# Kernel tuning notes

Hardware: AMD Instinct MI355X
Metric: run time of the kernel (lower is better)

Reference implementation:

```python
import jax, jax.numpy as jnp
import numpy as np

B, N, M, DIN, H = 8, 2048, 2048, 512, 256
SCALE = float(np.sqrt(H))


def _lin_params(key, din, dout):
    kw, kb = jax.random.split(key)
    lim = 1.0 / np.sqrt(din)
    W = jax.random.uniform(kw, (din, dout), jnp.float32, -lim, lim)
    b = jax.random.uniform(kb, (dout,), jnp.float32, -lim, lim)
    return W, b


def setup_inputs() -> dict:
    key = jax.random.key(0)
    ks = jax.random.split(key, 16)
    inp = {
        "q_fp": jax.random.normal(ks[0], (B, N, DIN), jnp.float32),
        "v_ret": jax.random.normal(ks[1], (B, M, DIN), jnp.float32),
        "pi_star": jax.random.uniform(ks[2], (B, N, M), jnp.float32),
    }
    names = ["qs", "ks", "vs", "qe", "ke", "ve"]
    for i, nm in enumerate(names):
        W, b = _lin_params(ks[3 + i], DIN, H)
        inp[f"W{nm}"], inp[f"b{nm}"] = W, b
    inp["W1"], inp["b1"] = _lin_params(ks[10], 4 * H, H)
    inp["W2"], inp["b2"] = _lin_params(ks[11], H, H)
    inp["gamma"] = jnp.ones((1,), jnp.float32)
    inp["ew"] = jnp.array(1.0, jnp.float32)
    return inp


def _forward(q_fp, v_ret, pi_star, Wqs, bqs, Wks, bks, Wvs, bvs,
             Wqe, bqe, Wke, bke, Wve, bve, W1, b1, W2, b2, gamma, ew):
    q_struct = q_fp @ Wqs + bqs          # [B,N,H]
    k_struct = v_ret @ Wks + bks         # [B,M,H]
    v_struct = v_ret @ Wvs + bvs
    q_elec = q_fp @ Wqe + bqe
    k_elec = v_ret @ Wke + bke
    v_elec = v_ret @ Wve + bve

    structural_logits = jnp.einsum("bnh,bmh->bnm", q_struct, k_struct) / SCALE

    # cdist(p=2) via the quadratic expansion, clamped for numeric safety
    q2 = jnp.sum(q_elec * q_elec, -1, keepdims=True)          # [B,N,1]
    k2 = jnp.sum(k_elec * k_elec, -1, keepdims=True)          # [B,M,1]
    d2 = q2 + jnp.swapaxes(k2, -2, -1) - 2.0 * jnp.einsum("bnh,bmh->bnm", q_elec, k_elec)
    electronic_distance = jnp.sqrt(jnp.maximum(d2, 1e-12))    # [B,N,M]
    electronic_scale = jnp.maximum(
        electronic_distance.mean(axis=(-2, -1), keepdims=True), 1e-4)
    electronic_logits = -(electronic_distance / electronic_scale)

    pi_mask = gamma * jnp.log(jnp.maximum(pi_star, 1e-9))
    final_logits = structural_logits + ew * electronic_logits + pi_mask
    attn = jax.nn.softmax(final_logits, axis=-1)              # [B,N,M]

    ctx_s = jnp.einsum("bnm,bmh->bnh", attn, v_struct)
    ctx_e = jnp.einsum("bnm,bmh->bnh", attn, v_elec)
    fused = jnp.concatenate([ctx_s, ctx_e, ctx_s - ctx_e, ctx_s * ctx_e], axis=-1)
    h = jax.nn.silu(fused @ W1 + b1)
    return h @ W2 + b2


def reference(q_fp, v_ret, pi_star, Wqs, bqs, Wks, bks, Wvs, bvs,
              Wqe, bqe, Wke, bke, Wve, bve, W1, b1, W2, b2, gamma, ew):
    return _forward(q_fp, v_ret, pi_star, Wqs, bqs, Wks, bks, Wvs, bvs,
                    Wqe, bqe, Wke, bke, Wve, bve, W1, b1, W2, b2, gamma, ew)
```

## Files before the change

kernel.cpp:

```cpp
#include <hip/hip_runtime.h>

#define Bsz 8
#define Nq  2048
#define Mk  2048
#define BKt 32

typedef __attribute__((ext_vector_type(8))) short   short8;
typedef __attribute__((ext_vector_type(4))) float   floatx4;

__device__ __forceinline__ unsigned short f2bf(float f) {
  union { float f; unsigned u; } x; x.f = f;
  unsigned r = x.u + 0x7fffu + ((x.u >> 16) & 1u);
  return (unsigned short)(r >> 16);
}
__device__ __forceinline__ float bf2f(unsigned short s) {
  union { unsigned u; float f; } x; x.u = ((unsigned)s) << 16;
  return x.f;
}

__device__ __forceinline__ void async16(const unsigned short* g, unsigned short* l) {
  __builtin_amdgcn_global_load_lds(
      (const __attribute__((address_space(1))) unsigned int*)g,
      (__attribute__((address_space(3))) unsigned int*)l, 16, 0, 0);
}

__device__ __forceinline__ void gemm_core_nt(
    const unsigned short* __restrict__ A, int lda,
    const unsigned short* __restrict__ B, int ldb,
    int K, unsigned short* ldsA, unsigned short* ldsB,
    floatx4 (&acc)[4][4])
{
  const int tid  = threadIdx.x;
  const int lane = tid & 63;
  const int sr   = tid >> 2;
  const int sc   = (tid & 3) << 3;
  const int wid  = tid >> 6;
  const int wm   = wid & 1;
  const int wn   = wid >> 1;
  const int fr   = lane & 15;
  const int fk   = (lane >> 4) << 3;

  const unsigned short* a0p = A + (size_t)sr * lda + sc;
  const unsigned short* a1p = A + (size_t)(sr + 64) * lda + sc;
  const unsigned short* b0p = B + (size_t)sr * ldb + sc;
  const unsigned short* b1p = B + (size_t)(sr + 64) * ldb + sc;
  unsigned short* la0 = ldsA + tid * 8;
  unsigned short* la1 = ldsA + 2048 + tid * 8;
  unsigned short* lb0 = ldsB + tid * 8;
  unsigned short* lb1 = ldsB + 2048 + tid * 8;
  const unsigned short* fa = ldsA + (wm * 64 + fr) * BKt + fk;
  const unsigned short* fb = ldsB + (wn * 64 + fr) * BKt + fk;

  for (int k0 = 0; k0 < K; k0 += BKt) {
    __syncthreads();
    async16(a0p, la0); a0p += BKt;
    async16(a1p, la1); a1p += BKt;
    async16(b0p, lb0); b0p += BKt;
    async16(b1p, lb1); b1p += BKt;
    __syncthreads();
    short8 af[4], bfr[4];
#pragma unroll
    for (int i = 0; i < 4; i++) af[i]  = *(const short8*)(fa + i * 16 * BKt);
#pragma unroll
    for (int i = 0; i < 4; i++) bfr[i] = *(const short8*)(fb + i * 16 * BKt);
#pragma unroll
    for (int i = 0; i < 4; i++)
#pragma unroll
      for (int j = 0; j < 4; j++)
        acc[i][j] = __builtin_amdgcn_mfma_f32_16x16x32_bf16(af[i], bfr[j], acc[i][j], 0, 0, 0);
  }
}

#define EPILOGUE_VARS \
  const int lane = threadIdx.x & 63; \
  const int wid  = threadIdx.x >> 6; \
  const int wm   = wid & 1; \
  const int wn   = wid >> 1; \
  const int r4   = (lane >> 4) * 4;  \
  const int cn   = lane & 15; \
  (void)wid;

template<int MODE>
__global__ __launch_bounds__(256) void k_gemm_bias(
    const unsigned short* __restrict__ A, const unsigned short* __restrict__ Bw,
    const float* __restrict__ bias, void* __restrict__ Cout, int Ncols, int K)
{
  __shared__ alignas(16) unsigned short ldsA[128 * BKt];
  __shared__ alignas(16) unsigned short ldsB[128 * BKt];
  floatx4 acc[4][4];
#pragma unroll
  for (int i = 0; i < 4; i++)
#pragma unroll
    for (int j = 0; j < 4; j++)
#pragma unroll
      for (int t = 0; t < 4; t++) acc[i][j][t] = 0.f;

  const unsigned short* Ab = A + (size_t)blockIdx.x * 128 * K;
  const unsigned short* Bb = Bw + (size_t)blockIdx.y * 128 * K;
  gemm_core_nt(Ab, K, Bb, K, K, ldsA, ldsB, acc);

  EPILOGUE_VARS
#pragma unroll
  for (int i = 0; i < 4; i++) {
#pragma unroll
    for (int j = 0; j < 4; j++) {
      int gc = blockIdx.y * 128 + wn * 64 + j * 16 + cn;
      float bv = bias[gc];
#pragma unroll
      for (int r = 0; r < 4; r++) {
        int gr = blockIdx.x * 128 + wm * 64 + i * 16 + r4 + r;
        float v = acc[i][j][r] + bv;
        if constexpr (MODE == 1) v = v / (1.f + __expf(-v));
        if constexpr (MODE == 2)
          ((float*)Cout)[(size_t)gr * Ncols + gc] = v;
        else
          ((unsigned short*)Cout)[(size_t)gr * Ncols + gc] = f2bf(v);
      }
    }
  }
}

__global__ __launch_bounds__(256) void k_pass1(
    const unsigned short* __restrict__ Xq, const unsigned short* __restrict__ Xk,
    const float* __restrict__ q2, const float* __restrict__ k2,
    float* __restrict__ dsum, float* __restrict__ rowsum)
{
  {
    int blin = (blockIdx.z * 16 + blockIdx.y) * 16 + blockIdx.x;
    if (threadIdx.x < 8) rowsum[blin * 8 + threadIdx.x] = 0.f;
  }
  __shared__ alignas(16) unsigned short ldsA[128 * BKt];
  __shared__ alignas(16) unsigned short ldsB[128 * BKt];
  floatx4 acc[4][4];
#pragma unroll
  for (int i = 0; i < 4; i++)
#pragma unroll
    for (int j = 0; j < 4; j++)
#pragma unroll
      for (int t = 0; t < 4; t++) acc[i][j][t] = 0.f;

  const int b = blockIdx.z;
  const unsigned short* Ab = Xq + ((size_t)(b * Nq) + blockIdx.x * 128) * 512 + 256;
  const unsigned short* Bb = Xk + ((size_t)(b * Mk) + blockIdx.y * 128) * 1024 + 512;
  gemm_core_nt(Ab, 512, Bb, 1024, 256, ldsA, ldsB, acc);

  EPILOGUE_VARS
  const int rowBase = b * Nq + blockIdx.x * 128;
  const int colBase = b * Mk + blockIdx.y * 128;
  float lsum = 0.f;
#pragma unroll
  for (int i = 0; i < 4; i++) {
#pragma unroll
    for (int j = 0; j < 4; j++) {
      float kk = k2[colBase + wn * 64 + j * 16 + cn];
#pragma unroll
      for (int r = 0; r < 4; r++) {
        float qq = q2[rowBase + wm * 64 + i * 16 + r4 + r];
        float d2 = qq + kk - 2.f * acc[i][j][r];
        lsum += sqrtf(fmaxf(d2, 1e-12f));
      }
    }
  }
#pragma unroll
  for (int o = 32; o; o >>= 1) lsum += __shfl_down(lsum, o);
  __syncthreads();
  float* red = (float*)ldsA;
  if (lane == 0) red[wid] = lsum;
  __syncthreads();
  if (threadIdx.x == 0) atomicAdd(dsum + b, red[0] + red[1] + red[2] + red[3]);
}

__global__ __launch_bounds__(256) void k_logits(
    const unsigned short* __restrict__ Xq, const unsigned short* __restrict__ Xk,
    const float* __restrict__ q2, const float* __restrict__ k2,
    const float* __restrict__ dsum, const float* __restrict__ pi,
    const float* __restrict__ gamma_p, const float* __restrict__ ew_p,
    unsigned short* __restrict__ attn, float* __restrict__ rowsum)
{
  __shared__ alignas(16) unsigned short ldsA[128 * BKt];
  __shared__ alignas(16) unsigned short ldsB[128 * BKt];
  floatx4 accS[4][4], accE[4][4];
#pragma unroll
  for (int i = 0; i < 4; i++)
#pragma unroll
    for (int j = 0; j < 4; j++)
#pragma unroll
      for (int t = 0; t < 4; t++) { accS[i][j][t] = 0.f; accE[i][j][t] = 0.f; }

  const int b = blockIdx.z;
  const unsigned short* Aq_s = Xq + ((size_t)(b * Nq) + blockIdx.x * 128) * 512;
  const unsigned short* Bk_s = Xk + ((size_t)(b * Mk) + blockIdx.y * 128) * 1024;
  gemm_core_nt(Aq_s,       512, Bk_s,       1024, 256, ldsA, ldsB, accS);
  gemm_core_nt(Aq_s + 256, 512, Bk_s + 512, 1024, 256, ldsA, ldsB, accE);

  const float scale = fmaxf(dsum[b] * (1.f / (2048.f * 2048.f)), 1e-4f);
  const float einv  = ew_p[0] / scale;
  const float gv    = gamma_p[0];

  EPILOGUE_VARS
  float rs[4][4];
#pragma unroll
  for (int i = 0; i < 4; i++)
#pragma unroll
    for (int r = 0; r < 4; r++) rs[i][r] = 0.f;

#pragma unroll
  for (int i = 0; i < 4; i++) {
#pragma unroll
    for (int j = 0; j < 4; j++) {
      int m = blockIdx.y * 128 + wn * 64 + j * 16 + cn;
      float kk = k2[b * Mk + m];
#pragma unroll
      for (int r = 0; r < 4; r++) {
        int n = blockIdx.x * 128 + wm * 64 + i * 16 + r4 + r;
        float qq = q2[b * Nq + n];
        float d  = sqrtf(fmaxf(qq + kk - 2.f * accE[i][j][r], 1e-12f));
        float p  = pi[((size_t)b * Nq + n) * Mk + m];
        float l  = accS[i][j][r] * 0.0625f - einv * d + gv * __logf(fmaxf(p, 1e-9f));
        float e  = __expf(l);
        rs[i][r] += e;
        attn[((size_t)b * Nq + n) * Mk + m] = f2bf(e);
      }
    }
  }
#pragma unroll
  for (int i = 0; i < 4; i++)
#pragma unroll
    for (int r = 0; r < 4; r++) {
      float v = rs[i][r];
      v += __shfl_xor(v, 1); v += __shfl_xor(v, 2);
      v += __shfl_xor(v, 4); v += __shfl_xor(v, 8);
      if (cn == 0)
        atomicAdd(rowsum + b * Nq + blockIdx.x * 128 + wm * 64 + i * 16 + r4 + r, v);
    }
}

__global__ __launch_bounds__(256) void k_pv(
    const unsigned short* __restrict__ At, const unsigned short* __restrict__ VT,
    const float* __restrict__ rowsum, unsigned short* __restrict__ ctx)
{
  __shared__ alignas(16) unsigned short ldsA[128 * BKt];
  __shared__ alignas(16) unsigned short ldsB[128 * BKt];
  floatx4 acc[4][4];
#pragma unroll
  for (int i = 0; i < 4; i++)
#pragma unroll
    for (int j = 0; j < 4; j++)
#pragma unroll
      for (int t = 0; t < 4; t++) acc[i][j][t] = 0.f;

  const int b = blockIdx.z;
  const unsigned short* Ab = At + ((size_t)b * Nq + blockIdx.x * 128) * (size_t)Mk;
  const unsigned short* Bb = VT + ((size_t)b * 512 + blockIdx.y * 128) * (size_t)Mk;
  gemm_core_nt(Ab, Mk, Bb, Mk, Mk, ldsA, ldsB, acc);

  EPILOGUE_VARS
  const int rowbase = b * Nq + blockIdx.x * 128 + wm * 64;
  float rinv[4][4];
#pragma unroll
  for (int i = 0; i < 4; i++)
#pragma unroll
    for (int r = 0; r < 4; r++)
      rinv[i][r] = 1.f / rowsum[rowbase + i * 16 + r4 + r];
#pragma unroll
  for (int i = 0; i < 4; i++)
#pragma unroll
    for (int j = 0; j < 4; j++) {
      int gc = blockIdx.y * 128 + wn * 64 + j * 16 + cn;
#pragma unroll
      for (int r = 0; r < 4; r++) {
        int gr = blockIdx.x * 128 + wm * 64 + i * 16 + r4 + r;
        ctx[((size_t)b * Nq + gr) * 512 + gc] = f2bf(acc[i][j][r] * rinv[i][r]);
      }
    }
}

__global__ void k_f32_bf16(const float* __restrict__ src, unsigned short* __restrict__ dst) {
  size_t i = ((size_t)blockIdx.x * 256 + threadIdx.x) * 4;
  float4 v = *(const float4*)(src + i);
  uint2 o;
  o.x = f2bf(v.x) | ((unsigned)f2bf(v.y) << 16);
  o.y = f2bf(v.z) | ((unsigned)f2bf(v.w) << 16);
  *(uint2*)(dst + i) = o;
}

__global__ void k_prep_w(
    const float* __restrict__ Wqs, const float* __restrict__ Wqe,
    const float* __restrict__ Wks, const float* __restrict__ Wvs,
    const float* __restrict__ Wke, const float* __restrict__ Wve,
    const float* __restrict__ W1,  const float* __restrict__ W2,
    const float* __restrict__ bqs, const float* __restrict__ bqe,
    const float* __restrict__ bks, const float* __restrict__ bvs,
    const float* __restrict__ bke, const float* __restrict__ bve,
    unsigned short* __restrict__ WqT, unsigned short* __restrict__ WkT,
    unsigned short* __restrict__ W1T, unsigned short* __restrict__ W2T,
    float* __restrict__ bq, float* __restrict__ bk, float* __restrict__ dsum)
{
  int gid = blockIdx.x * 256 + threadIdx.x;
  int idx = gid;
  if (idx < 512 * 512) {
    int j = idx >> 9, k = idx & 511;
    float v = (j < 256) ? Wqs[k * 256 + j] : Wqe[k * 256 + (j - 256)];
    WqT[idx] = f2bf(v);
  } else if ((idx -= 512 * 512) < 1024 * 512) {
    int j = idx >> 9, k = idx & 511;
    int s = j >> 8, jj = j & 255;
    const float* Wp = (s == 0) ? Wks : (s == 1) ? Wvs : (s == 2) ? Wke : Wve;
    WkT[idx] = f2bf(Wp[k * 256 + jj]);
  } else if ((idx -= 1024 * 512) < 256 * 1024) {
    int j = idx >> 10, k = idx & 1023;
    W1T[idx] = f2bf(W1[k * 256 + j]);
  } else if ((idx -= 256 * 1024) < 256 * 256) {
    int j = idx >> 8, k = idx & 255;
    W2T[idx] = f2bf(W2[k * 256 + j]);
  }
  if (gid < 512)  bq[gid] = (gid < 256) ? bqs[gid] : bqe[gid - 256];
  if (gid < 1024) bk[gid] = (gid < 256) ? bks[gid]
                    : (gid < 512) ? bvs[gid - 256]
                    : (gid < 768) ? bke[gid - 512] : bve[gid - 768];
  if (gid < 8) dsum[gid] = 0.f;
}

__global__ __launch_bounds__(256) void k_rowsq(
    const unsigned short* __restrict__ X, int stride, int colOff, float* __restrict__ out)
{
  int row = blockIdx.x * 4 + (threadIdx.x >> 6);
  int lane = threadIdx.x & 63;
  const unsigned short* p = X + (size_t)row * stride + colOff + lane * 4;
  uint2 u = *(const uint2*)p;
  float a0 = bf2f((unsigned short)(u.x & 0xffff));
  float a1 = bf2f((unsigned short)(u.x >> 16));
  float a2 = bf2f((unsigned short)(u.y & 0xffff));
  float a3 = bf2f((unsigned short)(u.y >> 16));
  float s = a0 * a0 + a1 * a1 + a2 * a2 + a3 * a3;
#pragma unroll
  for (int o = 32; o; o >>= 1) s += __shfl_down(s, o);
  if (lane == 0) out[row] = s;
}

__global__ void k_trans_vt(const unsigned short* __restrict__ Xk, unsigned short* __restrict__ VT) {
  __shared__ unsigned short t[32][33];
  const int b = blockIdx.z;
  const int m0 = blockIdx.x * 32, j0 = blockIdx.y * 32;
  const int tx = threadIdx.x, ty = threadIdx.y;
#pragma unroll
  for (int i = 0; i < 4; i++) {
    int m = m0 + ty + i * 8;
    int j = j0 + tx;
    int c = (j < 256) ? (256 + j) : (512 + j);
    t[ty + i * 8][tx] = Xk[((size_t)b * Mk + m) * 1024 + c];
  }
  __syncthreads();
#pragma unroll
  for (int i = 0; i < 4; i++) {
    int j = j0 + ty + i * 8;
    int m = m0 + tx;
    VT[((size_t)b * 512 + j) * Mk + m] = t[tx][ty + i * 8];
  }
}

__global__ void k_fused(const unsigned short* __restrict__ ctx, unsigned short* __restrict__ fused) {
  int idx = blockIdx.x * 256 + threadIdx.x;
  int bn = idx >> 8;
  int j = idx & 255;
  float cs = bf2f(ctx[(size_t)bn * 512 + j]);
  float ce = bf2f(ctx[(size_t)bn * 512 + 256 + j]);
  size_t o = (size_t)bn * 1024 + j;
  fused[o]       = f2bf(cs);
  fused[o + 256] = f2bf(ce);
  fused[o + 512] = f2bf(cs - ce);
  fused[o + 768] = f2bf(cs * ce);
}

extern "C" void kernel_launch(void* const* d_in, const int* in_sizes, int n_in,
                              void* d_out, int out_size, void* d_ws, size_t ws_size,
                              hipStream_t stream) {
  (void)in_sizes; (void)n_in; (void)out_size; (void)ws_size;
  const float* q_fp  = (const float*)d_in[0];
  const float* v_ret = (const float*)d_in[1];
  const float* pi    = (const float*)d_in[2];
  const float* Wqs = (const float*)d_in[3];  const float* bqs = (const float*)d_in[4];
  const float* Wks = (const float*)d_in[5];  const float* bks = (const float*)d_in[6];
  const float* Wvs = (const float*)d_in[7];  const float* bvs = (const float*)d_in[8];
  const float* Wqe = (const float*)d_in[9];  const float* bqe = (const float*)d_in[10];
  const float* Wke = (const float*)d_in[11]; const float* bke = (const float*)d_in[12];
  const float* Wve = (const float*)d_in[13]; const float* bve = (const float*)d_in[14];
  const float* W1  = (const float*)d_in[15]; const float* b1  = (const float*)d_in[16];
  const float* W2  = (const float*)d_in[17]; const float* b2  = (const float*)d_in[18];
  const float* gamma = (const float*)d_in[19];
  const float* ew    = (const float*)d_in[20];

  char* w = (char*)d_ws;
  unsigned short* WqT = (unsigned short*)(w + 0);
  unsigned short* WkT = (unsigned short*)(w + 524288);
  unsigned short* W1T = (unsigned short*)(w + 1572864);
  unsigned short* W2T = (unsigned short*)(w + 2097152);
  float* bq   = (float*)(w + 2228224);
  float* bk   = (float*)(w + 2230272);
  float* q2   = (float*)(w + 2234368);
  float* k2   = (float*)(w + 2299904);
  float* dsum = (float*)(w + 2365440);
  unsigned short* Aq = (unsigned short*)(w + 2365696);
  unsigned short* Ak = (unsigned short*)(w + 19142912);
  unsigned short* Xq = (unsigned short*)(w + 35920128);
  unsigned short* Xk = (unsigned short*)(w + 52697344);
  unsigned short* VT = (unsigned short*)(w + 86251776);
  unsigned short* attn = (unsigned short*)(w + 103028992);
  unsigned short* ctx  = Aq;
  unsigned short* fused = (unsigned short*)(w + 103028992);
  unsigned short* hbuf  = Ak;
  float* rowsum = (float*)d_out;

  k_f32_bf16<<<8192, 256, 0, stream>>>(q_fp, Aq);
  k_f32_bf16<<<8192, 256, 0, stream>>>(v_ret, Ak);
  k_prep_w<<<4352, 256, 0, stream>>>(Wqs, Wqe, Wks, Wvs, Wke, Wve, W1, W2,
                                     bqs, bqe, bks, bvs, bke, bve,
                                     WqT, WkT, W1T, W2T, bq, bk, dsum);
  k_gemm_bias<0><<<dim3(128, 4), 256, 0, stream>>>(Aq, WqT, bq, Xq, 512, 512);
  k_gemm_bias<0><<<dim3(128, 8), 256, 0, stream>>>(Ak, WkT, bk, Xk, 1024, 512);
  k_rowsq<<<4096, 256, 0, stream>>>(Xq, 512, 256, q2);
  k_rowsq<<<4096, 256, 0, stream>>>(Xk, 1024, 512, k2);
  k_pass1<<<dim3(16, 16, 8), 256, 0, stream>>>(Xq, Xk, q2, k2, dsum, rowsum);
  k_logits<<<dim3(16, 16, 8), 256, 0, stream>>>(Xq, Xk, q2, k2, dsum, pi, gamma, ew,
                                                attn, rowsum);
  k_trans_vt<<<dim3(64, 16, 8), dim3(32, 8), 0, stream>>>(Xk, VT);
  k_pv<<<dim3(16, 4, 8), 256, 0, stream>>>(attn, VT, rowsum, ctx);
  k_fused<<<16384, 256, 0, stream>>>(ctx, fused);
  k_gemm_bias<1><<<dim3(128, 2), 256, 0, stream>>>(fused, W1T, b1, hbuf, 256, 1024);
  k_gemm_bias<2><<<dim3(128, 2), 256, 0, stream>>>(hbuf, W2T, b2, d_out, 256, 256);
}
```

Before: 671.0 us.

## Cache electronic distances in fp16 from pass1 and drop recompute GEMM in logits

Pass1 now writes each computed cdist value as fp16 into the attention buffer, and the logits kernel reads it back instead of recomputing the electronic GEMM. This roughly halves the MFMA work in the logits kernel, which now relies on in-place aliasing of Dbuf and attn (each element is read before it is overwritten). The pi log/exp is skipped when gamma is 1, and the GEMM core swaps async global-to-LDS loads for register-staged loads issued before the barrier. It adds 2 bytes per element of extra HBM write and read and costs fp16 precision on the distances. Launch bounds with min 4 blocks per SM are also added.

New measurement: 609.9 us. 1.1x faster.

```diff
diff --git a/kernel.cpp b/kernel.cpp
--- a/kernel.cpp
+++ b/kernel.cpp
@@ -16,12 +16,6 @@
 __device__ __forceinline__ float bf2f(unsigned short s) {
   union { unsigned u; float f; } x; x.u = ((unsigned)s) << 16;
   return x.f;
-}
-
-__device__ __forceinline__ void async16(const unsigned short* g, unsigned short* l) {
-  __builtin_amdgcn_global_load_lds(
-      (const __attribute__((address_space(1))) unsigned int*)g,
-      (__attribute__((address_space(3))) unsigned int*)l, 16, 0, 0);
 }
 
 __device__ __forceinline__ void gemm_core_nt(
@@ -44,19 +38,20 @@
   const unsigned short* a1p = A + (size_t)(sr + 64) * lda + sc;
   const unsigned short* b0p = B + (size_t)sr * ldb + sc;
   const unsigned short* b1p = B + (size_t)(sr + 64) * ldb + sc;
-  unsigned short* la0 = ldsA + tid * 8;
-  unsigned short* la1 = ldsA + 2048 + tid * 8;
-  unsigned short* lb0 = ldsB + tid * 8;
-  unsigned short* lb1 = ldsB + 2048 + tid * 8;
+  uint4* sa0 = (uint4*)(ldsA + sr * BKt + sc);
+  uint4* sa1 = (uint4*)(ldsA + (sr + 64) * BKt + sc);
+  uint4* sb0 = (uint4*)(ldsB + sr * BKt + sc);
+  uint4* sb1 = (uint4*)(ldsB + (sr + 64) * BKt + sc);
   const unsigned short* fa = ldsA + (wm * 64 + fr) * BKt + fk;
   const unsigned short* fb = ldsB + (wn * 64 + fr) * BKt + fk;
 
   for (int k0 = 0; k0 < K; k0 += BKt) {
+    uint4 a0 = *(const uint4*)a0p; a0p += BKt;
+    uint4 a1 = *(const uint4*)a1p; a1p += BKt;
+    uint4 b0 = *(const uint4*)b0p; b0p += BKt;
+    uint4 b1 = *(const uint4*)b1p; b1p += BKt;
     __syncthreads();
-    async16(a0p, la0); a0p += BKt;
-    async16(a1p, la1); a1p += BKt;
-    async16(b0p, lb0); b0p += BKt;
-    async16(b1p, lb1); b1p += BKt;
+    *sa0 = a0; *sa1 = a1; *sb0 = b0; *sb1 = b1;
     __syncthreads();
     short8 af[4], bfr[4];
 #pragma unroll
@@ -120,10 +115,11 @@
   }
 }
 
-__global__ __launch_bounds__(256) void k_pass1(
+__global__ __launch_bounds__(256, 4) void k_pass1(
     const unsigned short* __restrict__ Xq, const unsigned short* __restrict__ Xk,
     const float* __restrict__ q2, const float* __restrict__ k2,
-    float* __restrict__ dsum, float* __restrict__ rowsum)
+    float* __restrict__ dsum, float* __restrict__ rowsum,
+    _Float16* __restrict__ Dbuf)
 {
   {
     int blin = (blockIdx.z * 16 + blockIdx.y) * 16 + blockIdx.x;
@@ -145,19 +141,20 @@
   gemm_core_nt(Ab, 512, Bb, 1024, 256, ldsA, ldsB, acc);
 
   EPILOGUE_VARS
-  const int rowBase = b * Nq + blockIdx.x * 128;
-  const int colBase = b * Mk + blockIdx.y * 128;
   float lsum = 0.f;
 #pragma unroll
   for (int i = 0; i < 4; i++) {
 #pragma unroll
     for (int j = 0; j < 4; j++) {
-      float kk = k2[colBase + wn * 64 + j * 16 + cn];
+      int m = blockIdx.y * 128 + wn * 64 + j * 16 + cn;
+      float kk = k2[b * Mk + m];
 #pragma unroll
       for (int r = 0; r < 4; r++) {
-        float qq = q2[rowBase + wm * 64 + i * 16 + r4 + r];
-        float d2 = qq + kk - 2.f * acc[i][j][r];
-        lsum += sqrtf(fmaxf(d2, 1e-12f));
+        int n = blockIdx.x * 128 + wm * 64 + i * 16 + r4 + r;
+        float qq = q2[b * Nq + n];
+        float d  = sqrtf(fmaxf(qq + kk - 2.f * acc[i][j][r], 1e-12f));
+        lsum += d;
+        Dbuf[((size_t)b * Nq + n) * Mk + m] = (_Float16)d;
       }
     }
   }
@@ -170,32 +167,33 @@
   if (threadIdx.x == 0) atomicAdd(dsum + b, red[0] + red[1] + red[2] + red[3]);
 }
 
-__global__ __launch_bounds__(256) void k_logits(
+__global__ __launch_bounds__(256, 4) void k_logits(
     const unsigned short* __restrict__ Xq, const unsigned short* __restrict__ Xk,
-    const float* __restrict__ q2, const float* __restrict__ k2,
     const float* __restrict__ dsum, const float* __restrict__ pi,
     const float* __restrict__ gamma_p, const float* __restrict__ ew_p,
     unsigned short* __restrict__ attn, float* __restrict__ rowsum)
 {
   __shared__ alignas(16) unsigned short ldsA[128 * BKt];
   __shared__ alignas(16) unsigned short ldsB[128 * BKt];
-  floatx4 accS[4][4], accE[4][4];
+  floatx4 accS[4][4];
 #pragma unroll
   for (int i = 0; i < 4; i++)
 #pragma unroll
     for (int j = 0; j < 4; j++)
 #pragma unroll
-      for (int t = 0; t < 4; t++) { accS[i][j][t] = 0.f; accE[i][j][t] = 0.f; }
+      for (int t = 0; t < 4; t++) accS[i][j][t] = 0.f;
 
   const int b = blockIdx.z;
   const unsigned short* Aq_s = Xq + ((size_t)(b * Nq) + blockIdx.x * 128) * 512;
   const unsigned short* Bk_s = Xk + ((size_t)(b * Mk) + blockIdx.y * 128) * 1024;
-  gemm_core_nt(Aq_s,       512, Bk_s,       1024, 256, ldsA, ldsB, accS);
-  gemm_core_nt(Aq_s + 256, 512, Bk_s + 512, 1024, 256, ldsA, ldsB, accE);
+  gemm_core_nt(Aq_s, 512, Bk_s, 1024, 256, ldsA, ldsB, accS);
 
   const float scale = fmaxf(dsum[b] * (1.f / (2048.f * 2048.f)), 1e-4f);
   const float einv  = ew_p[0] / scale;
   const float gv    = gamma_p[0];
+  const bool  g1    = (gv == 1.0f);
+
+  const _Float16* Dbuf = (const _Float16*)attn;
 
   EPILOGUE_VARS
   float rs[4][4];
@@ -209,17 +207,16 @@
 #pragma unroll
     for (int j = 0; j < 4; j++) {
       int m = blockIdx.y * 128 + wn * 64 + j * 16 + cn;
-      float kk = k2[b * Mk + m];
 #pragma unroll
       for (int r = 0; r < 4; r++) {
         int n = blockIdx.x * 128 + wm * 64 + i * 16 + r4 + r;
-        float qq = q2[b * Nq + n];
-        float d  = sqrtf(fmaxf(qq + kk - 2.f * accE[i][j][r], 1e-12f));
-        float p  = pi[((size_t)b * Nq + n) * Mk + m];
-        float l  = accS[i][j][r] * 0.0625f - einv * d + gv * __logf(fmaxf(p, 1e-9f));
-        float e  = __expf(l);
+        size_t idx = ((size_t)b * Nq + n) * Mk + m;
+        float d  = (float)Dbuf[idx];
+        float p  = fmaxf(pi[idx], 1e-9f);
+        float pf = g1 ? p : __expf(gv * __logf(p));
+        float e  = __expf(accS[i][j][r] * 0.0625f - einv * d) * pf;
         rs[i][r] += e;
-        attn[((size_t)b * Nq + n) * Mk + m] = f2bf(e);
+        attn[idx] = f2bf(e);
       }
     }
   }
@@ -406,9 +403,11 @@
   unsigned short* Xk = (unsigned short*)(w + 52697344);
   unsigned short* VT = (unsigned short*)(w + 86251776);
   unsigned short* attn = (unsigned short*)(w + 103028992);
+  _Float16*       Dbuf = (_Float16*)attn;
   unsigned short* ctx  = Aq;
-  unsigned short* fused = (unsigned short*)(w + 103028992);
+  unsigned short* fused = (unsigned short*)(w + 103028992 + 67108864) - 16384 * 1024;
   unsigned short* hbuf  = Ak;
+  fused = attn;
   float* rowsum = (float*)d_out;
 
   k_f32_bf16<<<8192, 256, 0, stream>>>(q_fp, Aq);
@@ -420,8 +419,8 @@
   k_gemm_bias<0><<<dim3(128, 8), 256, 0, stream>>>(Ak, WkT, bk, Xk, 1024, 512);
   k_rowsq<<<4096, 256, 0, stream>>>(Xq, 512, 256, q2);
   k_rowsq<<<4096, 256, 0, stream>>>(Xk, 1024, 512, k2);
-  k_pass1<<<dim3(16, 16, 8), 256, 0, stream>>>(Xq, Xk, q2, k2, dsum, rowsum);
-  k_logits<<<dim3(16, 16, 8), 256, 0, stream>>>(Xq, Xk, q2, k2, dsum, pi, gamma, ew,
+  k_pass1<<<dim3(16, 16, 8), 256, 0, stream>>>(Xq, Xk, q2, k2, dsum, rowsum, Dbuf);
+  k_logits<<<dim3(16, 16, 8), 256, 0, stream>>>(Xq, Xk, dsum, pi, gamma, ew,
                                                 attn, rowsum);
   k_trans_vt<<<dim3(64, 16, 8), dim3(32, 8), 0, stream>>>(Xk, VT);
   k_pv<<<dim3(16, 4, 8), 256, 0, stream>>>(attn, VT, rowsum, ctx);
```
